# Optimization experiments

Measured on AMD Instinct MI355X. Metric: run time of the kernel, lower is better.

The kernel has to match this reference:

```python
import jax, jax.numpy as jnp
import numpy as np
from math import sqrt

B, L = 2, 1024
D, H, DH = 768, 12, 64
NL, FF = 4, 3072
V, CTX, EOS = 50257, 1024, 50256
STD = 0.02


def setup_inputs() -> dict:
    key = jax.random.key(0)
    ks = jax.random.split(key, 16)
    std_o = STD / sqrt(NL)  # init scales rows==d_model by 1/sqrt(num_layers)
    return {
        'input_ids': jax.random.randint(ks[0], (B, L), 0, V),
        'token_emb': jax.random.normal(ks[1], (V, D), jnp.float32) * STD,
        'pos_emb': jax.random.normal(ks[2], (CTX, D), jnp.float32) * STD,
        'ln1_g': jnp.ones((NL, D), jnp.float32),
        'ln1_b': jnp.zeros((NL, D), jnp.float32),
        'Wq': jax.random.normal(ks[3], (NL, H, D, DH), jnp.float32) * STD,
        'bq': jnp.zeros((NL, H, DH), jnp.float32),
        'Wk': jax.random.normal(ks[4], (NL, H, D, DH), jnp.float32) * STD,
        'bk': jnp.zeros((NL, H, DH), jnp.float32),
        'Wv': jax.random.normal(ks[5], (NL, H, D, DH), jnp.float32) * STD,
        'bv': jnp.zeros((NL, H, DH), jnp.float32),
        'Wo': jax.random.normal(ks[6], (NL, D, D), jnp.float32) * std_o,
        'bo': jnp.zeros((NL, D), jnp.float32),
        'ln2_g': jnp.ones((NL, D), jnp.float32),
        'ln2_b': jnp.zeros((NL, D), jnp.float32),
        'W1': jax.random.normal(ks[7], (NL, D, FF), jnp.float32) * STD,
        'b1': jnp.zeros((NL, FF), jnp.float32),
        'W2': jax.random.normal(ks[8], (NL, FF, D), jnp.float32) * std_o,
        'b2': jnp.zeros((NL, D), jnp.float32),
    }


def _layernorm(x, g, b, eps=1e-5):
    m = jnp.mean(x, axis=-1, keepdims=True)
    v = jnp.mean(jnp.square(x - m), axis=-1, keepdims=True)
    return (x - m) * jax.lax.rsqrt(v + eps) * g + b


def _packed_supporters(input_ids):
    b, l = input_ids.shape
    raw = jnp.broadcast_to(jnp.arange(l), (b, l))
    last_eos = jax.lax.cummax(jnp.where(input_ids == EOS, raw, 0), axis=1)
    rel_idx = raw - last_eos
    seg = jnp.cumsum((input_ids == EOS).astype(jnp.int32), axis=1)
    same_seg = seg[:, :, None] == seg[:, None, :]
    causal = jnp.tril(jnp.ones((l, l), bool))
    mask = jnp.where(same_seg & causal, 0.0, -jnp.inf).astype(jnp.float32)  # [B,L,L]
    return rel_idx, mask


def reference(input_ids, token_emb, pos_emb, ln1_g, ln1_b, Wq, bq, Wk, bk, Wv, bv,
              Wo, bo, ln2_g, ln2_b, W1, b1, W2, b2):
    b, l = input_ids.shape
    d = token_emb.shape[1]
    rel_idx, mask = _packed_supporters(input_ids)
    x = token_emb[input_ids] * sqrt(d) + pos_emb[rel_idx]  # [B,L,D]
    for i in range(Wq.shape[0]):
        # --- attention sub-block (pre-LN, residual) ---
        h = _layernorm(x, ln1_g[i], ln1_b[i])
        q = jnp.einsum('bld,hdk->bhlk', h, Wq[i]) + bq[i][None, :, None, :]
        k = jnp.einsum('bld,hdk->bhlk', h, Wk[i]) + bk[i][None, :, None, :]
        v = jnp.einsum('bld,hdk->bhlk', h, Wv[i]) + bv[i][None, :, None, :]
        # NOTE: original has NO 1/sqrt(d_head) scaling
        logits = jnp.einsum('bhlk,bhmk->bhlm', q, k) + mask[:, None, :, :]
        w = jax.nn.softmax(logits, axis=-1)
        o = jnp.einsum('bhlm,bhmk->bhlk', w, v)
        o = o.transpose(0, 2, 1, 3).reshape(b, l, d)  # concat heads
        x = x + (o @ Wo[i] + bo[i])
        # --- MLP sub-block ---
        h = _layernorm(x, ln2_g[i], ln2_b[i])
        h = jax.nn.gelu(h @ W1[i] + b1[i], approximate=False)
        x = x + (h @ W2[i] + b2[i])
    return x @ token_emb.T  # tied decoder, no bias
```

## Files before the change

### kernel.cpp

```cpp
#include <hip/hip_runtime.h>

typedef unsigned short u16;
typedef unsigned int u32;
typedef __bf16 bf16x8 __attribute__((ext_vector_type(8)));
typedef float f32x4 __attribute__((ext_vector_type(4)));

#define EOS_ID 50256
#define DM 768
#define NH 12
#define DHD 64
#define SEQ 1024
#define NB 2
#define NLAYERS 4
#define DFF 3072
#define NV 50257
#define NVP 50304
#define NTOK 2048
#define QKVW 2304

__device__ __forceinline__ float bf2f(u16 u) {
  union { float f; u32 u; } x; x.u = ((u32)u) << 16; return x.f;
}
__device__ __forceinline__ u16 f2bf(float f) {
  union { float f; u32 u; } x; x.f = f;
  u32 u = x.u;
  u += 0x7fffu + ((u >> 16) & 1u);
  return (u16)(u >> 16);
}
__device__ __forceinline__ u32 pack2(float a, float b) {
  return (u32)f2bf(a) | ((u32)f2bf(b) << 16);
}

__device__ __forceinline__ void gload16(const u16* g, u16* l) {
  __builtin_amdgcn_global_load_lds(
      (const __attribute__((address_space(1))) unsigned int*)g,
      (__attribute__((address_space(3))) unsigned int*)l, 16, 0, 0);
}

__global__ __launch_bounds__(1024)
void scan_kernel(const int* __restrict__ ids, int* __restrict__ rel, int* __restrict__ seg) {
  __shared__ int sm[1024];
  __shared__ int ss[1024];
  const int b = blockIdx.x, t = threadIdx.x;
  const int e = (ids[b * SEQ + t] == EOS_ID) ? 1 : 0;
  sm[t] = e ? t : 0;
  ss[t] = e;
  __syncthreads();
  for (int o = 1; o < 1024; o <<= 1) {
    int vm = 0, vs = 0;
    if (t >= o) { vm = sm[t - o]; vs = ss[t - o]; }
    __syncthreads();
    if (t >= o) { if (vm > sm[t]) sm[t] = vm; ss[t] += vs; }
    __syncthreads();
  }
  rel[b * SEQ + t] = t - sm[t];
  seg[b * SEQ + t] = ss[t];
}

__global__ __launch_bounds__(256)
void embed_kernel(const int* __restrict__ ids, const int* __restrict__ rel,
                  const float* __restrict__ tok, const float* __restrict__ pos,
                  float* __restrict__ x) {
  const int row = blockIdx.x;
  const int id = ids[row];
  const int r = rel[row];
  const float s = 27.712812921102035f;
  for (int d = threadIdx.x; d < DM; d += 256)
    x[(size_t)row * DM + d] = tok[(size_t)id * DM + d] * s + pos[(size_t)r * DM + d];
}

__global__ __launch_bounds__(256)
void tok2bf_kernel(const float* __restrict__ tok, u16* __restrict__ out) {
  const size_t i = ((size_t)blockIdx.x * 256 + threadIdx.x) * 8;
  if (i >= (size_t)NVP * DM) return;
  const size_t row = i / DM;
  uint4 o;
  if (row < NV) {
    const float4 f0 = *(const float4*)(tok + i);
    const float4 f1 = *(const float4*)(tok + i + 4);
    o = make_uint4(pack2(f0.x, f0.y), pack2(f0.z, f0.w), pack2(f1.x, f1.y), pack2(f1.z, f1.w));
  } else {
    o = make_uint4(0, 0, 0, 0);
  }
  *(uint4*)(out + i) = o;
}

__global__ __launch_bounds__(256)
void ln_kernel(const float* __restrict__ x, const float* __restrict__ g,
               const float* __restrict__ b, u16* __restrict__ out) {
  const int row = blockIdx.x, t = threadIdx.x;
  const int wave = t >> 6, lane = t & 63;
  const float* xr = x + (size_t)row * DM;
  float v0 = xr[t], v1 = xr[t + 256], v2 = xr[t + 512];
  __shared__ float red[4];
  float s = v0 + v1 + v2;
  for (int o = 32; o; o >>= 1) s += __shfl_down(s, o, 64);
  if (lane == 0) red[wave] = s;
  __syncthreads();
  const float mean = (red[0] + red[1] + red[2] + red[3]) * (1.f / DM);
  __syncthreads();
  const float a0 = v0 - mean, a1 = v1 - mean, a2 = v2 - mean;
  float s2 = a0 * a0 + a1 * a1 + a2 * a2;
  for (int o = 32; o; o >>= 1) s2 += __shfl_down(s2, o, 64);
  if (lane == 0) red[wave] = s2;
  __syncthreads();
  const float var = (red[0] + red[1] + red[2] + red[3]) * (1.f / DM);
  const float rstd = rsqrtf(var + 1e-5f);
  u16* orow = out + (size_t)row * DM;
  orow[t]       = f2bf(a0 * rstd * g[t]       + b[t]);
  orow[t + 256] = f2bf(a1 * rstd * g[t + 256] + b[t + 256]);
  orow[t + 512] = f2bf(a2 * rstd * g[t + 512] + b[t + 512]);
}

__global__ __launch_bounds__(256)
void repack_qkv(const float* __restrict__ Wq, const float* __restrict__ Wk,
                const float* __restrict__ Wv, int layer, u16* __restrict__ out) {
  const int idx = blockIdx.x * 256 + threadIdx.x;
  if (idx >= QKVW * DM) return;
  const int n = idx / DM, k = idx % DM;
  const int sel = n / DM;
  const int hh = (n % DM) / DHD, dh = n % DHD;
  const float* W = (sel == 0) ? Wq : (sel == 1) ? Wk : Wv;
  out[idx] = f2bf(W[(((size_t)layer * NH + hh) * DM + k) * DHD + dh]);
}

__global__ __launch_bounds__(256)
void repack_bias(const float* __restrict__ bq, const float* __restrict__ bk,
                 const float* __restrict__ bv, int layer, float* __restrict__ out) {
  const int n = blockIdx.x * 256 + threadIdx.x;
  if (n >= QKVW) return;
  const int sel = n / DM;
  const int hh = (n % DM) / DHD, dh = n % DHD;
  const float* B = (sel == 0) ? bq : (sel == 1) ? bk : bv;
  out[n] = B[((size_t)layer * NH + hh) * DHD + dh];
}

__global__ __launch_bounds__(256)
void transpose_f2b(const float* __restrict__ src, u16* __restrict__ dst, int R, int C) {
  __shared__ float tile[32][33];
  const int c0 = blockIdx.x * 32, r0 = blockIdx.y * 32;
  const int tx = threadIdx.x & 31, ty = threadIdx.x >> 5;
  for (int i = 0; i < 32; i += 8)
    tile[ty + i][tx] = src[(size_t)(r0 + ty + i) * C + c0 + tx];
  __syncthreads();
  for (int i = 0; i < 32; i += 8)
    dst[(size_t)(c0 + ty + i) * R + r0 + tx] = f2bf(tile[tx][ty + i]);
}

__global__ __launch_bounds__(256)
void f2bf_kernel(const float* __restrict__ in, u16* __restrict__ out, int n) {
  const int i = blockIdx.x * 256 + threadIdx.x;
  if (i < n) out[i] = f2bf(in[i]);
}

template <int EPI>
__global__ __launch_bounds__(256)
void gemm_bt(const u16* __restrict__ A, const u16* __restrict__ BT,
             const float* __restrict__ bias, void* __restrict__ out,
             const int M, const int N, const int K) {
  __shared__ u16 As[128 * 32];
  __shared__ u16 Bs[128 * 32];
  const int t = threadIdx.x;
  const int wave = t >> 6, lane = t & 63;
  const int l15 = lane & 15, quad = lane >> 4;
  const int wm = wave >> 1, wn = wave & 1;
  const int m0 = blockIdx.y * 128;
  const int n0 = blockIdx.x * 128;

  const int rsub = lane >> 2;
  const int cseg = (lane & 3) * 8;
  const u16* gA0 = A + (size_t)(m0 + wave * 32 + rsub) * K + cseg;
  const u16* gA1 = gA0 + (size_t)16 * K;
  const u16* gB0 = BT + (size_t)(n0 + wave * 32 + rsub) * K + cseg;
  const u16* gB1 = gB0 + (size_t)16 * K;
  u16* lA0 = &As[(wave * 32) * 32];
  u16* lA1 = &As[(wave * 32 + 16) * 32];
  u16* lB0 = &Bs[(wave * 32) * 32];
  u16* lB1 = &Bs[(wave * 32 + 16) * 32];

  f32x4 acc[4][4] = {};

  for (int k0 = 0; k0 < K; k0 += 32) {
    __syncthreads();
    gload16(gA0 + k0, lA0);
    gload16(gA1 + k0, lA1);
    gload16(gB0 + k0, lB0);
    gload16(gB1 + k0, lB1);
    __syncthreads();
    bf16x8 af[4], bfr[4];
#pragma unroll
    for (int mt = 0; mt < 4; mt++)
      af[mt] = *(const bf16x8*)&As[(wm * 64 + mt * 16 + l15) * 32 + quad * 8];
#pragma unroll
    for (int nt = 0; nt < 4; nt++)
      bfr[nt] = *(const bf16x8*)&Bs[(wn * 64 + nt * 16 + l15) * 32 + quad * 8];
#pragma unroll
    for (int mt = 0; mt < 4; mt++)
#pragma unroll
      for (int nt = 0; nt < 4; nt++)
        acc[mt][nt] = __builtin_amdgcn_mfma_f32_16x16x32_bf16(af[mt], bfr[nt], acc[mt][nt], 0, 0, 0);
  }

#pragma unroll
  for (int nt = 0; nt < 4; nt++) {
    const int n = n0 + wn * 64 + nt * 16 + l15;
    const float bvv = bias ? bias[n] : 0.f;
#pragma unroll
    for (int mt = 0; mt < 4; mt++) {
      const int mb = m0 + wm * 64 + mt * 16 + quad * 4;
#pragma unroll
      for (int r = 0; r < 4; r++) {
        const size_t idx = (size_t)(mb + r) * N + n;
        const float v = acc[mt][nt][r] + bvv;
        if (EPI == 0) {
          ((u16*)out)[idx] = f2bf(v);
        } else if (EPI == 1) {
          ((float*)out)[idx] += v;
        } else {
          const float gg = 0.5f * v * (1.f + erff(v * 0.70710678118654752f));
          ((u16*)out)[idx] = f2bf(gg);
        }
      }
    }
  }
}

__global__ __launch_bounds__(256)
void gemm_final(const u16* __restrict__ A, const u16* __restrict__ BT,
                float* __restrict__ out, const int M, const int N, const int K) {
  __shared__ float smem_f[4224];
  u16* As = (u16*)smem_f;
  u16* Bs = (u16*)smem_f + 128 * 32;

  const int t = threadIdx.x;
  const int wave = t >> 6, lane = t & 63;
  const int l15 = lane & 15, quad = lane >> 4;
  const int wm = wave >> 1, wn = wave & 1;

  const int bid = blockIdx.x;
  const int nper = gridDim.x >> 3;
  const int gt = (bid & 7) * nper + (bid >> 3);
  const int mtile = gt & 15;
  const int ntile = gt >> 4;
  const int m0 = mtile * 128;
  const int n0 = ntile * 128;

  const int rsub = lane >> 2;
  const int cseg = (lane & 3) * 8;
  const u16* gA0 = A + (size_t)(m0 + wave * 32 + rsub) * K + cseg;
  const u16* gA1 = gA0 + (size_t)16 * K;
  const u16* gB0 = BT + (size_t)(n0 + wave * 32 + rsub) * K + cseg;
  const u16* gB1 = gB0 + (size_t)16 * K;
  u16* lA0 = &As[(wave * 32) * 32];
  u16* lA1 = &As[(wave * 32 + 16) * 32];
  u16* lB0 = &Bs[(wave * 32) * 32];
  u16* lB1 = &Bs[(wave * 32 + 16) * 32];

  f32x4 acc[4][4] = {};

  for (int k0 = 0; k0 < K; k0 += 32) {
    __syncthreads();
    gload16(gA0 + k0, lA0);
    gload16(gA1 + k0, lA1);
    gload16(gB0 + k0, lB0);
    gload16(gB1 + k0, lB1);
    __syncthreads();
    bf16x8 af[4], bfr[4];
#pragma unroll
    for (int mt = 0; mt < 4; mt++)
      af[mt] = *(const bf16x8*)&As[(wm * 64 + mt * 16 + l15) * 32 + quad * 8];
#pragma unroll
    for (int nt = 0; nt < 4; nt++)
      bfr[nt] = *(const bf16x8*)&Bs[(wn * 64 + nt * 16 + l15) * 32 + quad * 8];
#pragma unroll
    for (int mt = 0; mt < 4; mt++)
#pragma unroll
      for (int nt = 0; nt < 4; nt++)
        acc[mt][nt] = __builtin_amdgcn_mfma_f32_16x16x32_bf16(af[mt], bfr[nt], acc[mt][nt], 0, 0, 0);
  }

  float* sc = smem_f;
  for (int mt = 0; mt < 4; mt++) {
    __syncthreads();
#pragma unroll
    for (int nt = 0; nt < 4; nt++)
#pragma unroll
      for (int r = 0; r < 4; r++)
        sc[(wm * 16 + quad * 4 + r) * 132 + wn * 64 + nt * 16 + l15] = acc[mt][nt][r];
    __syncthreads();
#pragma unroll
    for (int it = 0; it < 16; it++) {
      const int lin = it * 256 + t;
      const int s = lin >> 7;
      const int c = lin & 127;
      const int grow = m0 + mt * 16 + (s & 15) + (s >> 4) * 64;
      const int gcol = n0 + c;
      if (gcol < N) out[(size_t)grow * N + gcol] = sc[s * 132 + c];
    }
  }
}

__global__ __launch_bounds__(256)
void attn_kernel(const u16* __restrict__ qkv, const int* __restrict__ seg,
                 u16* __restrict__ ob) {
  __shared__ int seg_lds[SEQ];
  __shared__ u16 VT[64 * 40];
  __shared__ u16 PL[4][16 * 40];

  const int t = threadIdx.x;
  const int wave = t >> 6, lane = t & 63;
  const int l15 = lane & 15, quad = lane >> 4;
  const int bid = blockIdx.x;
  const int qb = bid & 15;
  const int hh = (bid >> 4) % NH;
  const int b = (bid >> 4) / NH;
  const size_t rowbase = (size_t)b * SEQ;
  const int kvmax = (qb + 1) * 64;
  const int qw0 = qb * 64 + wave * 16;

  for (int idx = t; idx < kvmax; idx += 256) seg_lds[idx] = seg[b * SEQ + idx];

  const u16* qrow = qkv + (rowbase + qw0 + l15) * QKVW + hh * DHD;
  const bf16x8 qf0 = *(const bf16x8*)(qrow + quad * 8);
  const bf16x8 qf1 = *(const bf16x8*)(qrow + 32 + quad * 8);

  __syncthreads();
  const int si = seg_lds[qw0 + l15];

  const int vkv = t >> 3;
  const int vdd = (t & 7) * 8;
  const u16* vbase = qkv + rowbase * QKVW + 2 * DM + hh * DHD + vdd;
  const u16* kbase = qkv + rowbase * QKVW + DM + hh * DHD;

  uint4 vld = *(const uint4*)(vbase + (size_t)vkv * QKVW);
  uint4 kfa = *(const uint4*)(kbase + (size_t)l15 * QKVW + quad * 8);
  uint4 kfb = *(const uint4*)(kbase + (size_t)l15 * QKVW + 32 + quad * 8);
  uint4 kfc = *(const uint4*)(kbase + (size_t)(16 + l15) * QKVW + quad * 8);
  uint4 kfd = *(const uint4*)(kbase + (size_t)(16 + l15) * QKVW + 32 + quad * 8);

  f32x4 o0 = {}, o1 = {}, o2 = {}, o3 = {};
  float mrun = -1e30f, lrun = 0.f;

  const int nch = kvmax >> 5;
  for (int c = 0; c < nch; c++) {
    const int j0 = c << 5;
    __syncthreads();
    {
      const u16* pv = (const u16*)&vld;
#pragma unroll
      for (int jj = 0; jj < 8; jj++) VT[(vdd + jj) * 40 + vkv] = pv[jj];
    }
    __syncthreads();
    const int j1 = (c + 1 < nch) ? j0 + 32 : j0;
    uint4 vld_n = *(const uint4*)(vbase + (size_t)(j1 + vkv) * QKVW);
    uint4 kfa_n = *(const uint4*)(kbase + (size_t)(j1 + l15) * QKVW + quad * 8);
    uint4 kfb_n = *(const uint4*)(kbase + (size_t)(j1 + l15) * QKVW + 32 + quad * 8);
    uint4 kfc_n = *(const uint4*)(kbase + (size_t)(j1 + 16 + l15) * QKVW + quad * 8);
    uint4 kfd_n = *(const uint4*)(kbase + (size_t)(j1 + 16 + l15) * QKVW + 32 + quad * 8);

    f32x4 s0 = {}, s1 = {};
    s0 = __builtin_amdgcn_mfma_f32_16x16x32_bf16(*(const bf16x8*)&kfa, qf0, s0, 0, 0, 0);
    s0 = __builtin_amdgcn_mfma_f32_16x16x32_bf16(*(const bf16x8*)&kfb, qf1, s0, 0, 0, 0);
    s1 = __builtin_amdgcn_mfma_f32_16x16x32_bf16(*(const bf16x8*)&kfc, qf0, s1, 0, 0, 0);
    s1 = __builtin_amdgcn_mfma_f32_16x16x32_bf16(*(const bf16x8*)&kfd, qf1, s1, 0, 0, 0);

    const int iq = qw0 + l15;
    float p[8];
    float cmax = -1e30f;
#pragma unroll
    for (int r = 0; r < 4; r++) {
      int j = j0 + quad * 4 + r;
      bool ok = (j <= iq) && (seg_lds[j] == si);
      float sv = ok ? s0[r] : -1e30f;
      p[r] = sv; cmax = fmaxf(cmax, sv);
      j += 16;
      ok = (j <= iq) && (seg_lds[j] == si);
      sv = ok ? s1[r] : -1e30f;
      p[4 + r] = sv; cmax = fmaxf(cmax, sv);
    }
    cmax = fmaxf(cmax, __shfl_xor(cmax, 16, 64));
    cmax = fmaxf(cmax, __shfl_xor(cmax, 32, 64));
    const float mnew = fmaxf(mrun, cmax);
    const float fsc = __expf(mrun - mnew);
    mrun = mnew;
    float csum = 0.f;
#pragma unroll
    for (int r = 0; r < 8; r++) {
      const float e = (p[r] > -5e29f) ? __expf(p[r] - mnew) : 0.f;
      p[r] = e; csum += e;
    }
    csum += __shfl_xor(csum, 16, 64);
    csum += __shfl_xor(csum, 32, 64);
    lrun = lrun * fsc + csum;
#pragma unroll
    for (int r = 0; r < 4; r++) { o0[r] *= fsc; o1[r] *= fsc; o2[r] *= fsc; o3[r] *= fsc; }

    u32* plw = (u32*)&PL[wave][l15 * 40 + quad * 4];
    plw[0] = pack2(p[0], p[1]);
    plw[1] = pack2(p[2], p[3]);
    u32* plw2 = (u32*)&PL[wave][l15 * 40 + 16 + quad * 4];
    plw2[0] = pack2(p[4], p[5]);
    plw2[1] = pack2(p[6], p[7]);

    const bf16x8 pf = *(const bf16x8*)&PL[wave][l15 * 40 + quad * 8];
    const bf16x8 va = *(const bf16x8*)&VT[(l15) * 40 + quad * 8];
    const bf16x8 vb = *(const bf16x8*)&VT[(16 + l15) * 40 + quad * 8];
    const bf16x8 vc = *(const bf16x8*)&VT[(32 + l15) * 40 + quad * 8];
    const bf16x8 vd8 = *(const bf16x8*)&VT[(48 + l15) * 40 + quad * 8];
    o0 = __builtin_amdgcn_mfma_f32_16x16x32_bf16(va, pf, o0, 0, 0, 0);
    o1 = __builtin_amdgcn_mfma_f32_16x16x32_bf16(vb, pf, o1, 0, 0, 0);
    o2 = __builtin_amdgcn_mfma_f32_16x16x32_bf16(vc, pf, o2, 0, 0, 0);
    o3 = __builtin_amdgcn_mfma_f32_16x16x32_bf16(vd8, pf, o3, 0, 0, 0);

    vld = vld_n; kfa = kfa_n; kfb = kfb_n; kfc = kfc_n; kfd = kfd_n;
  }

  const float inv = 1.f / lrun;
  u16* orow = ob + (rowbase + qw0 + l15) * DM + hh * DHD;
#pragma unroll
  for (int r = 0; r < 4; r++) {
    orow[quad * 4 + r]      = f2bf(o0[r] * inv);
    orow[16 + quad * 4 + r] = f2bf(o1[r] * inv);
    orow[32 + quad * 4 + r] = f2bf(o2[r] * inv);
    orow[48 + quad * 4 + r] = f2bf(o3[r] * inv);
  }
}

static inline void launch_gemm(int epi, const u16* A, const u16* BT, const float* bias,
                               void* out, int M, int N, int K, hipStream_t s) {
  dim3 g(N / 128, M / 128);
  if (epi == 0)      gemm_bt<0><<<g, 256, 0, s>>>(A, BT, bias, out, M, N, K);
  else if (epi == 1) gemm_bt<1><<<g, 256, 0, s>>>(A, BT, bias, out, M, N, K);
  else               gemm_bt<2><<<g, 256, 0, s>>>(A, BT, bias, out, M, N, K);
}

extern "C" void kernel_launch(void* const* d_in, const int* in_sizes, int n_in,
                              void* d_out, int out_size, void* d_ws, size_t ws_size,
                              hipStream_t stream) {
  (void)in_sizes; (void)n_in; (void)out_size; (void)ws_size;
  const int*   ids  = (const int*)d_in[0];
  const float* tok  = (const float*)d_in[1];
  const float* pos  = (const float*)d_in[2];
  const float* ln1g = (const float*)d_in[3];
  const float* ln1b = (const float*)d_in[4];
  const float* Wq   = (const float*)d_in[5];
  const float* bq   = (const float*)d_in[6];
  const float* Wk   = (const float*)d_in[7];
  const float* bk   = (const float*)d_in[8];
  const float* Wv   = (const float*)d_in[9];
  const float* bv   = (const float*)d_in[10];
  const float* Wo   = (const float*)d_in[11];
  const float* bo   = (const float*)d_in[12];
  const float* ln2g = (const float*)d_in[13];
  const float* ln2b = (const float*)d_in[14];
  const float* W1   = (const float*)d_in[15];
  const float* b1   = (const float*)d_in[16];
  const float* W2   = (const float*)d_in[17];
  const float* b2   = (const float*)d_in[18];

  char* w = (char*)d_ws;
  auto carve = [&](size_t bytes) -> char* {
    char* p = w;
    w += (bytes + 255) & ~(size_t)255;
    return p;
  };
  int*   rel  = (int*)carve((size_t)NTOK * 4);
  int*   seg  = (int*)carve((size_t)NTOK * 4);
  float* x    = (float*)carve((size_t)NTOK * DM * 4);
  u16*   hb   = (u16*)carve((size_t)NTOK * DM * 2);
  u16*   qkvb = (u16*)carve((size_t)NTOK * QKVW * 2);
  u16*   ob   = (u16*)carve((size_t)NTOK * DM * 2);
  u16*   ffb  = (u16*)carve((size_t)NTOK * DFF * 2);
  u16*   Wqkv = (u16*)carve((size_t)QKVW * DM * 2);
  float* bqkv = (float*)carve((size_t)QKVW * 4);
  u16*   WoT  = (u16*)carve((size_t)DM * DM * 2);
  u16*   W1T  = (u16*)carve((size_t)DFF * DM * 2);
  u16*   W2T  = (u16*)carve((size_t)DM * DFF * 2);
  u16*   tokb = (u16*)carve((size_t)NVP * DM * 2);

  scan_kernel<<<NB, 1024, 0, stream>>>(ids, rel, seg);
  embed_kernel<<<NTOK, 256, 0, stream>>>(ids, rel, tok, pos, x);
  tok2bf_kernel<<<(int)(((size_t)NVP * DM / 8 + 255) / 256), 256, 0, stream>>>(tok, tokb);

  for (int i = 0; i < NLAYERS; i++) {
    ln_kernel<<<NTOK, 256, 0, stream>>>(x, ln1g + (size_t)i * DM, ln1b + (size_t)i * DM, hb);
    repack_qkv<<<(QKVW * DM + 255) / 256, 256, 0, stream>>>(Wq, Wk, Wv, i, Wqkv);
    repack_bias<<<(QKVW + 255) / 256, 256, 0, stream>>>(bq, bk, bv, i, bqkv);
    launch_gemm(0, hb, Wqkv, bqkv, qkvb, NTOK, QKVW, DM, stream);
    attn_kernel<<<NB * NH * (SEQ / 64), 256, 0, stream>>>(qkvb, seg, ob);
    transpose_f2b<<<dim3(DM / 32, DM / 32), 256, 0, stream>>>(Wo + (size_t)i * DM * DM, WoT, DM, DM);
    launch_gemm(1, ob, WoT, bo + (size_t)i * DM, x, NTOK, DM, DM, stream);
    ln_kernel<<<NTOK, 256, 0, stream>>>(x, ln2g + (size_t)i * DM, ln2b + (size_t)i * DM, hb);
    transpose_f2b<<<dim3(DFF / 32, DM / 32), 256, 0, stream>>>(W1 + (size_t)i * DM * DFF, W1T, DM, DFF);
    launch_gemm(2, hb, W1T, b1 + (size_t)i * DFF, ffb, NTOK, DFF, DM, stream);
    transpose_f2b<<<dim3(DM / 32, DFF / 32), 256, 0, stream>>>(W2 + (size_t)i * DFF * DM, W2T, DFF, DM);
    launch_gemm(1, ffb, W2T, b2 + (size_t)i * DM, x, NTOK, DM, DFF, stream);
  }

  f2bf_kernel<<<(NTOK * DM + 255) / 256, 256, 0, stream>>>(x, hb, NTOK * DM);
  gemm_final<<<dim3((NTOK / 128) * (NVP / 128)), 256, 0, stream>>>(hb, tokb, (float*)d_out, NTOK, NV, DM);
}
```

Before: 1.827 ms.

## Double-buffer LDS tiles in GEMMs and tile-transpose the QKV weight repack

Both the generic GEMM and the final vocab GEMM now use two LDS buffers, issuing global-to-LDS loads for the next K-tile before computing on the current one, with explicit vmcnt waits and barriers. This is meant to hide global load latency behind the MFMA work. The QKV weight repack becomes a 32x32 shared-memory tiled transpose so that both reads and writes are coalesced, replacing the strided gather. The cost is doubled LDS use per block, which may reduce occupancy, and the correctness of the hand-placed waitcnt depends on how gload16 is implemented.

After: 1.734 ms. 5.1% less time.

```diff
diff --git a/kernel.cpp b/kernel.cpp
--- a/kernel.cpp
+++ b/kernel.cpp
@@ -115,13 +115,20 @@
 __global__ __launch_bounds__(256)
 void repack_qkv(const float* __restrict__ Wq, const float* __restrict__ Wk,
                 const float* __restrict__ Wv, int layer, u16* __restrict__ out) {
-  const int idx = blockIdx.x * 256 + threadIdx.x;
-  if (idx >= QKVW * DM) return;
-  const int n = idx / DM, k = idx % DM;
-  const int sel = n / DM;
-  const int hh = (n % DM) / DHD, dh = n % DHD;
-  const float* W = (sel == 0) ? Wq : (sel == 1) ? Wk : Wv;
-  out[idx] = f2bf(W[(((size_t)layer * NH + hh) * DM + k) * DHD + dh]);
+  __shared__ float tile[32][33];
+  const int z = blockIdx.z;
+  const int sel = z / NH, hh = z % NH;
+  const float* W = ((sel == 0) ? Wq : (sel == 1) ? Wk : Wv) +
+                   ((size_t)layer * NH + hh) * DM * DHD;
+  const int k0 = blockIdx.y * 32;
+  const int d0 = blockIdx.x * 32;
+  const int tx = threadIdx.x & 31, ty = threadIdx.x >> 5;
+  for (int i = 0; i < 32; i += 8)
+    tile[ty + i][tx] = W[(size_t)(k0 + ty + i) * DHD + d0 + tx];
+  __syncthreads();
+  u16* dst = out + ((size_t)sel * DM + hh * DHD + d0) * DM + k0;
+  for (int i = 0; i < 32; i += 8)
+    dst[(size_t)(ty + i) * DM + tx] = f2bf(tile[tx][ty + i]);
 }
 
 __global__ __launch_bounds__(256)
@@ -158,8 +165,8 @@
 void gemm_bt(const u16* __restrict__ A, const u16* __restrict__ BT,
              const float* __restrict__ bias, void* __restrict__ out,
              const int M, const int N, const int K) {
-  __shared__ u16 As[128 * 32];
-  __shared__ u16 Bs[128 * 32];
+  __shared__ u16 As[2][128 * 32];
+  __shared__ u16 Bs[2][128 * 32];
   const int t = threadIdx.x;
   const int wave = t >> 6, lane = t & 63;
   const int l15 = lane & 15, quad = lane >> 4;
@@ -173,37 +180,50 @@
   const u16* gA1 = gA0 + (size_t)16 * K;
   const u16* gB0 = BT + (size_t)(n0 + wave * 32 + rsub) * K + cseg;
   const u16* gB1 = gB0 + (size_t)16 * K;
-  u16* lA0 = &As[(wave * 32) * 32];
-  u16* lA1 = &As[(wave * 32 + 16) * 32];
-  u16* lB0 = &Bs[(wave * 32) * 32];
-  u16* lB1 = &Bs[(wave * 32 + 16) * 32];
 
   f32x4 acc[4][4] = {};
-
-  for (int k0 = 0; k0 < K; k0 += 32) {
-    __syncthreads();
-    gload16(gA0 + k0, lA0);
-    gload16(gA1 + k0, lA1);
-    gload16(gB0 + k0, lB0);
-    gload16(gB1 + k0, lB1);
-    __syncthreads();
+  const int nt = K >> 5;
+
+  gload16(gA0, &As[0][(wave * 32) * 32]);
+  gload16(gA1, &As[0][(wave * 32 + 16) * 32]);
+  gload16(gB0, &Bs[0][(wave * 32) * 32]);
+  gload16(gB1, &Bs[0][(wave * 32 + 16) * 32]);
+
+  int cur = 0;
+  for (int tt = 0; tt < nt; tt++) {
+    if (tt + 1 < nt) {
+      const int k1 = (tt + 1) << 5;
+      const int nb = cur ^ 1;
+      gload16(gA0 + k1, &As[nb][(wave * 32) * 32]);
+      gload16(gA1 + k1, &As[nb][(wave * 32 + 16) * 32]);
+      gload16(gB0 + k1, &Bs[nb][(wave * 32) * 32]);
+      gload16(gB1 + k1, &Bs[nb][(wave * 32 + 16) * 32]);
+      asm volatile("s_waitcnt vmcnt(4)" ::: "memory");
+    } else {
+      asm volatile("s_waitcnt vmcnt(0)" ::: "memory");
+    }
+    __builtin_amdgcn_s_barrier();
+    __builtin_amdgcn_sched_barrier(0);
     bf16x8 af[4], bfr[4];
 #pragma unroll
     for (int mt = 0; mt < 4; mt++)
-      af[mt] = *(const bf16x8*)&As[(wm * 64 + mt * 16 + l15) * 32 + quad * 8];
-#pragma unroll
-    for (int nt = 0; nt < 4; nt++)
-      bfr[nt] = *(const bf16x8*)&Bs[(wn * 64 + nt * 16 + l15) * 32 + quad * 8];
+      af[mt] = *(const bf16x8*)&As[cur][(wm * 64 + mt * 16 + l15) * 32 + quad * 8];
+#pragma unroll
+    for (int nn = 0; nn < 4; nn++)
+      bfr[nn] = *(const bf16x8*)&Bs[cur][(wn * 64 + nn * 16 + l15) * 32 + quad * 8];
 #pragma unroll
     for (int mt = 0; mt < 4; mt++)
 #pragma unroll
-      for (int nt = 0; nt < 4; nt++)
-        acc[mt][nt] = __builtin_amdgcn_mfma_f32_16x16x32_bf16(af[mt], bfr[nt], acc[mt][nt], 0, 0, 0);
-  }
-
-#pragma unroll
-  for (int nt = 0; nt < 4; nt++) {
-    const int n = n0 + wn * 64 + nt * 16 + l15;
+      for (int nn = 0; nn < 4; nn++)
+        acc[mt][nn] = __builtin_amdgcn_mfma_f32_16x16x32_bf16(af[mt], bfr[nn], acc[mt][nn], 0, 0, 0);
+    __builtin_amdgcn_sched_barrier(0);
+    __builtin_amdgcn_s_barrier();
+    cur ^= 1;
+  }
+
+#pragma unroll
+  for (int nn = 0; nn < 4; nn++) {
+    const int n = n0 + wn * 64 + nn * 16 + l15;
     const float bvv = bias ? bias[n] : 0.f;
 #pragma unroll
     for (int mt = 0; mt < 4; mt++) {
@@ -211,7 +231,7 @@
 #pragma unroll
       for (int r = 0; r < 4; r++) {
         const size_t idx = (size_t)(mb + r) * N + n;
-        const float v = acc[mt][nt][r] + bvv;
+        const float v = acc[mt][nn][r] + bvv;
         if (EPI == 0) {
           ((u16*)out)[idx] = f2bf(v);
         } else if (EPI == 1) {
@@ -228,10 +248,7 @@
 __global__ __launch_bounds__(256)
 void gemm_final(const u16* __restrict__ A, const u16* __restrict__ BT,
                 float* __restrict__ out, const int M, const int N, const int K) {
-  __shared__ float smem_f[4224];
-  u16* As = (u16*)smem_f;
-  u16* Bs = (u16*)smem_f + 128 * 32;
-
+  __shared__ u16 smem[2][2][128 * 32];
   const int t = threadIdx.x;
   const int wave = t >> 6, lane = t & 63;
   const int l15 = lane & 15, quad = lane >> 4;
@@ -251,42 +268,55 @@
   const u16* gA1 = gA0 + (size_t)16 * K;
   const u16* gB0 = BT + (size_t)(n0 + wave * 32 + rsub) * K + cseg;
   const u16* gB1 = gB0 + (size_t)16 * K;
-  u16* lA0 = &As[(wave * 32) * 32];
-  u16* lA1 = &As[(wave * 32 + 16) * 32];
-  u16* lB0 = &Bs[(wave * 32) * 32];
-  u16* lB1 = &Bs[(wave * 32 + 16) * 32];
 
   f32x4 acc[4][4] = {};
-
-  for (int k0 = 0; k0 < K; k0 += 32) {
-    __syncthreads();
-    gload16(gA0 + k0, lA0);
-    gload16(gA1 + k0, lA1);
-    gload16(gB0 + k0, lB0);
-    gload16(gB1 + k0, lB1);
-    __syncthreads();
+  const int nt = K >> 5;
+
+  gload16(gA0, &smem[0][0][(wave * 32) * 32]);
+  gload16(gA1, &smem[0][0][(wave * 32 + 16) * 32]);
+  gload16(gB0, &smem[1][0][(wave * 32) * 32]);
+  gload16(gB1, &smem[1][0][(wave * 32 + 16) * 32]);
+
+  int cur = 0;
+  for (int tt = 0; tt < nt; tt++) {
+    if (tt + 1 < nt) {
+      const int k1 = (tt + 1) << 5;
+      const int nb = cur ^ 1;
+      gload16(gA0 + k1, &smem[0][nb][(wave * 32) * 32]);
+      gload16(gA1 + k1, &smem[0][nb][(wave * 32 + 16) * 32]);
+      gload16(gB0 + k1, &smem[1][nb][(wave * 32) * 32]);
+      gload16(gB1 + k1, &smem[1][nb][(wave * 32 + 16) * 32]);
+      asm volatile("s_waitcnt vmcnt(4)" ::: "memory");
+    } else {
+      asm volatile("s_waitcnt vmcnt(0)" ::: "memory");
+    }
+    __builtin_amdgcn_s_barrier();
+    __builtin_amdgcn_sched_barrier(0);
     bf16x8 af[4], bfr[4];
 #pragma unroll
     for (int mt = 0; mt < 4; mt++)
-      af[mt] = *(const bf16x8*)&As[(wm * 64 + mt * 16 + l15) * 32 + quad * 8];
-#pragma unroll
-    for (int nt = 0; nt < 4; nt++)
-      bfr[nt] = *(const bf16x8*)&Bs[(wn * 64 + nt * 16 + l15) * 32 + quad * 8];
+      af[mt] = *(const bf16x8*)&smem[0][cur][(wm * 64 + mt * 16 + l15) * 32 + quad * 8];
+#pragma unroll
+    for (int nn = 0; nn < 4; nn++)
+      bfr[nn] = *(const bf16x8*)&smem[1][cur][(wn * 64 + nn * 16 + l15) * 32 + quad * 8];
 #pragma unroll
     for (int mt = 0; mt < 4; mt++)
 #pragma unroll
-      for (int nt = 0; nt < 4; nt++)
-        acc[mt][nt] = __builtin_amdgcn_mfma_f32_16x16x32_bf16(af[mt], bfr[nt], acc[mt][nt], 0, 0, 0);
-  }
-
-  float* sc = smem_f;
+      for (int nn = 0; nn < 4; nn++)
+        acc[mt][nn] = __builtin_amdgcn_mfma_f32_16x16x32_bf16(af[mt], bfr[nn], acc[mt][nn], 0, 0, 0);
+    __builtin_amdgcn_sched_barrier(0);
+    __builtin_amdgcn_s_barrier();
+    cur ^= 1;
+  }
+
+  float* sc = (float*)smem;
   for (int mt = 0; mt < 4; mt++) {
     __syncthreads();
 #pragma unroll
-    for (int nt = 0; nt < 4; nt++)
+    for (int nn = 0; nn < 4; nn++)
 #pragma unroll
       for (int r = 0; r < 4; r++)
-        sc[(wm * 16 + quad * 4 + r) * 132 + wn * 64 + nt * 16 + l15] = acc[mt][nt][r];
+        sc[(wm * 16 + quad * 4 + r) * 132 + wn * 64 + nn * 16 + l15] = acc[mt][nn][r];
     __syncthreads();
 #pragma unroll
     for (int it = 0; it < 16; it++) {
@@ -484,7 +514,7 @@
 
   for (int i = 0; i < NLAYERS; i++) {
     ln_kernel<<<NTOK, 256, 0, stream>>>(x, ln1g + (size_t)i * DM, ln1b + (size_t)i * DM, hb);
-    repack_qkv<<<(QKVW * DM + 255) / 256, 256, 0, stream>>>(Wq, Wk, Wv, i, Wqkv);
+    repack_qkv<<<dim3(DHD / 32, DM / 32, 3 * NH), 256, 0, stream>>>(Wq, Wk, Wv, i, Wqkv);
     repack_bias<<<(QKVW + 255) / 256, 256, 0, stream>>>(bq, bk, bv, i, bqkv);
     launch_gemm(0, hb, Wqkv, bqkv, qkvb, NTOK, QKVW, DM, stream);
     attn_kernel<<<NB * NH * (SEQ / 64), 256, 0, stream>>>(qkvb, seg, ob);
```
